# Kernel tuning notes

Hardware: AMD Instinct MI355X
Metric: run time of the kernel (lower is better)

The kernel has to match this reference:

```python
import jax, jax.numpy as jnp
import numpy as np

N, T, D = 128, 2048, 88

def setup_inputs() -> dict:
    key = jax.random.key(0)
    k1, k2 = jax.random.split(key)
    output = jax.random.normal(k1, (N, T, D), dtype=jnp.float32)
    # binary piano-roll style target (sparse note activations)
    target = (jax.random.uniform(k2, (N, T, D)) < 0.1).astype(jnp.float32)
    mask = jnp.ones((N, T), dtype=jnp.int32)  # left-aligned valid mask
    return {"output": output, "target": target, "mask": mask}

def reference(output, target, mask):
    # prediction = (sigmoid(output) > 0.5) -> non-differentiable 0/1 floats
    pred = (jax.nn.sigmoid(output) > 0.5).astype(output.dtype)
    # tru_pos summed over both feature and time dims -> [N]
    tru_pos = jnp.sum(pred * target, axis=(1, 2))
    # per-timestep false pos / false neg -> [N, T]
    false_pos = jnp.sum(pred * (1.0 - target), axis=2)
    false_neg = jnp.sum((1.0 - pred) * target, axis=2)
    # T_i = number of valid timesteps per sequence (loop runs over t < T_i)
    T_i = jnp.sum(mask, axis=1)  # [N] int
    valid = (jnp.arange(false_pos.shape[1])[None, :] < T_i[:, None]).astype(output.dtype)
    ratio = tru_pos[:, None] / (tru_pos[:, None] + false_pos + false_neg)  # [N, T]
    acc = jnp.sum(ratio * valid, axis=1) / T_i.astype(output.dtype)  # [N]
    return jnp.sum(acc)
```

## Files before the change

kernel.cpp:

```cpp
#include <hip/hip_runtime.h>
#include <stdint.h>

#define NN 128
#define TT 2048
#define DD 88
#define ROWS 32
#define F4_ROW 22
#define K1_BLOCKS (NN * TT / ROWS)
#define PARTS_PER_N (TT / ROWS)
#define CPN 8
#define K2_BLOCKS (NN * CPN)

typedef float f4 __attribute__((ext_vector_type(4)));

__global__ __launch_bounds__(256) void acc_rowstats_kernel(
    const float* __restrict__ outp, const float* __restrict__ tgt,
    float* __restrict__ fpfn, float* __restrict__ tp_part) {
  __shared__ float s_tp[4];

  const int tid = threadIdx.x;
  const int lane = tid & 63;
  const int wave = tid >> 6;
  const int blk = blockIdx.x;
  const size_t base = (size_t)blk * (ROWS * DD);

  const int r = tid >> 3;
  const int s = tid & 7;

  const f4* o4 = (const f4*)(outp + base) + (size_t)r * F4_ROW;
  const f4* g4 = (const f4*)(tgt + base) + (size_t)r * F4_ROW;

  const int j2 = (s < 6) ? (s + 16) : s;
  const f4 o0 = o4[s];
  const f4 g0 = g4[s];
  const f4 o1 = o4[s + 8];
  const f4 g1 = g4[s + 8];
  const f4 o2 = o4[j2];
  const f4 g2 = g4[j2];

  float x = 0.f, tp = 0.f;
  float x2 = 0.f, tp2 = 0.f;

#define ACC1(ov, gv, xa, ta)                        \
  do {                                              \
    const float pf = ((ov) > 0.f) ? 1.f : 0.f;      \
    (xa) += fabsf(pf - (gv));                       \
    (ta) = fmaf(pf, (gv), (ta));                    \
  } while (0)

  ACC1(o0.x, g0.x, x, tp); ACC1(o0.y, g0.y, x, tp);
  ACC1(o0.z, g0.z, x, tp); ACC1(o0.w, g0.w, x, tp);
  ACC1(o1.x, g1.x, x, tp); ACC1(o1.y, g1.y, x, tp);
  ACC1(o1.z, g1.z, x, tp); ACC1(o1.w, g1.w, x, tp);
  ACC1(o2.x, g2.x, x2, tp2); ACC1(o2.y, g2.y, x2, tp2);
  ACC1(o2.z, g2.z, x2, tp2); ACC1(o2.w, g2.w, x2, tp2);
#undef ACC1

  if (s < 6) { x += x2; tp += tp2; }

  x += __shfl_down(x, 4, 64);
  x += __shfl_down(x, 2, 64);
  x += __shfl_down(x, 1, 64);
  if (s == 0) fpfn[(size_t)blk * ROWS + r] = x;

  for (int off = 32; off > 0; off >>= 1) tp += __shfl_down(tp, off, 64);
  if (lane == 0) s_tp[wave] = tp;
  __syncthreads();
  if (tid == 0) tp_part[blk] = s_tp[0] + s_tp[1] + s_tp[2] + s_tp[3];
}

__global__ __launch_bounds__(256) void acc_chunk_kernel(
    const int* __restrict__ mask, const float* __restrict__ fpfn,
    const float* __restrict__ tp_part, float* __restrict__ accp) {
  const int b = blockIdx.x;
  const int n = b >> 3;
  const int c = b & (CPN - 1);
  const int tid = threadIdx.x;
  const int lane = tid & 63;
  const int wave = tid >> 6;
  __shared__ float s_ti[4];
  __shared__ float s_tp[4];
  __shared__ float s_a[4];

  const int4* m4 = (const int4*)(mask + (size_t)n * TT);
  const int4 v0 = m4[tid];
  const int4 v1 = m4[tid + 256];
  const float tpv = (tid < PARTS_PER_N) ? tp_part[n * PARTS_PER_N + tid] : 0.f;
  const int t = c * 256 + tid;
  const float fr = fpfn[(size_t)n * TT + t];

  int ti = v0.x + v0.y + v0.z + v0.w + v1.x + v1.y + v1.z + v1.w;
  float tp = tpv;
  for (int off = 32; off > 0; off >>= 1) {
    ti += __shfl_down(ti, off, 64);
    tp += __shfl_down(tp, off, 64);
  }
  if (lane == 0) { s_ti[wave] = (float)ti; s_tp[wave] = tp; }
  __syncthreads();
  const float fTi = s_ti[0] + s_ti[1] + s_ti[2] + s_ti[3];
  const float tpn = s_tp[0] + s_tp[1] + s_tp[2] + s_tp[3];
  const int Ti = (int)fTi;

  float a = (t < Ti) ? tpn / (tpn + fr) : 0.f;
  for (int off = 32; off > 0; off >>= 1) a += __shfl_down(a, off, 64);
  if (lane == 0) s_a[wave] = a;
  __syncthreads();
  if (tid == 0)
    accp[b] = (s_a[0] + s_a[1] + s_a[2] + s_a[3]) / fTi;
}

__global__ __launch_bounds__(256) void acc_sum_kernel(
    const float* __restrict__ accp, float* __restrict__ out) {
  const int tid = threadIdx.x;
  const int lane = tid & 63;
  const int wave = tid >> 6;
  __shared__ float s_a[4];
  float a = accp[tid] + accp[tid + 256] + accp[tid + 512] + accp[tid + 768];
  for (int off = 32; off > 0; off >>= 1) a += __shfl_down(a, off, 64);
  if (lane == 0) s_a[wave] = a;
  __syncthreads();
  if (tid == 0) out[0] = s_a[0] + s_a[1] + s_a[2] + s_a[3];
}

extern "C" void kernel_launch(void* const* d_in, const int* in_sizes, int n_in,
                              void* d_out, int out_size, void* d_ws, size_t ws_size,
                              hipStream_t stream) {
  const float* output = (const float*)d_in[0];
  const float* target = (const float*)d_in[1];
  const int* mask = (const int*)d_in[2];
  float* out = (float*)d_out;

  float* tp_part = (float*)d_ws;
  float* fpfn = tp_part + K1_BLOCKS;
  float* accp = fpfn + (size_t)NN * TT;

  acc_rowstats_kernel<<<K1_BLOCKS, 256, 0, stream>>>(output, target, fpfn, tp_part);
  acc_chunk_kernel<<<K2_BLOCKS, 256, 0, stream>>>(mask, fpfn, tp_part, accp);
  acc_sum_kernel<<<1, 256, 0, stream>>>(accp, out);
}
```

Baseline: 201.9 us.

## Process four tiles per block with double-buffered loads and per-wave TP partials

Each block of the row-stats kernel now handles four 32-row tiles instead of one. It software-pipelines the loads so the next tile's data is in flight while the current tile is reduced. The per-block shared-memory reduction and __syncthreads are dropped in favour of per-wave true-positive partials written to global memory, and the chunk kernel now reads 256 partials per sequence instead of 64. This cuts the block count and exposes more memory-level parallelism per thread, at the cost of more registers and a larger partial array.

```diff
diff --git a/kernel.cpp b/kernel.cpp
--- a/kernel.cpp
+++ b/kernel.cpp
@@ -6,8 +6,10 @@
 #define DD 88
 #define ROWS 32
 #define F4_ROW 22
-#define K1_BLOCKS (NN * TT / ROWS)
-#define PARTS_PER_N (TT / ROWS)
+#define TILES (NN * TT / ROWS)
+#define TILES_PER_BLK 4
+#define K1_GRID (TILES / TILES_PER_BLK)
+#define PARTS_PER_N 256
 #define CPN 8
 #define K2_BLOCKS (NN * CPN)
 
@@ -16,57 +18,65 @@
 __global__ __launch_bounds__(256) void acc_rowstats_kernel(
     const float* __restrict__ outp, const float* __restrict__ tgt,
     float* __restrict__ fpfn, float* __restrict__ tp_part) {
-  __shared__ float s_tp[4];
-
   const int tid = threadIdx.x;
   const int lane = tid & 63;
   const int wave = tid >> 6;
-  const int blk = blockIdx.x;
-  const size_t base = (size_t)blk * (ROWS * DD);
-
   const int r = tid >> 3;
   const int s = tid & 7;
+  const int j2 = (s < 6) ? (s + 16) : s;
+  const int tile0 = blockIdx.x * TILES_PER_BLK;
 
-  const f4* o4 = (const f4*)(outp + base) + (size_t)r * F4_ROW;
-  const f4* g4 = (const f4*)(tgt + base) + (size_t)r * F4_ROW;
+  const f4* __restrict__ ob = (const f4*)outp;
+  const f4* __restrict__ gb = (const f4*)tgt;
 
-  const int j2 = (s < 6) ? (s + 16) : s;
-  const f4 o0 = o4[s];
-  const f4 g0 = g4[s];
-  const f4 o1 = o4[s + 8];
-  const f4 g1 = g4[s + 8];
-  const f4 o2 = o4[j2];
-  const f4 g2 = g4[j2];
-
-  float x = 0.f, tp = 0.f;
-  float x2 = 0.f, tp2 = 0.f;
-
-#define ACC1(ov, gv, xa, ta)                        \
-  do {                                              \
-    const float pf = ((ov) > 0.f) ? 1.f : 0.f;      \
-    (xa) += fabsf(pf - (gv));                       \
-    (ta) = fmaf(pf, (gv), (ta));                    \
+#define LOADT(T, oA, gA, oB, gB, oC, gC)              \
+  do {                                                \
+    const size_t ro = ((size_t)(T) * ROWS + r) * F4_ROW; \
+    oA = ob[ro + s];      gA = gb[ro + s];            \
+    oB = ob[ro + s + 8];  gB = gb[ro + s + 8];        \
+    oC = ob[ro + j2];     gC = gb[ro + j2];           \
   } while (0)
 
-  ACC1(o0.x, g0.x, x, tp); ACC1(o0.y, g0.y, x, tp);
-  ACC1(o0.z, g0.z, x, tp); ACC1(o0.w, g0.w, x, tp);
-  ACC1(o1.x, g1.x, x, tp); ACC1(o1.y, g1.y, x, tp);
-  ACC1(o1.z, g1.z, x, tp); ACC1(o1.w, g1.w, x, tp);
-  ACC1(o2.x, g2.x, x2, tp2); ACC1(o2.y, g2.y, x2, tp2);
-  ACC1(o2.z, g2.z, x2, tp2); ACC1(o2.w, g2.w, x2, tp2);
+#define ACC1(ov, gv, xa, ta)                          \
+  do {                                                \
+    const float pf = ((ov) > 0.f) ? 1.f : 0.f;        \
+    (xa) += fabsf(pf - (gv));                         \
+    (ta) = fmaf(pf, (gv), (ta));                      \
+  } while (0)
+
+#define COMPT(T, oA, gA, oB, gB, oC, gC)                                   \
+  do {                                                                     \
+    float x = 0.f, tp = 0.f, x2 = 0.f, tp2 = 0.f;                          \
+    ACC1(oA.x, gA.x, x, tp);   ACC1(oA.y, gA.y, x, tp);                    \
+    ACC1(oA.z, gA.z, x, tp);   ACC1(oA.w, gA.w, x, tp);                    \
+    ACC1(oB.x, gB.x, x, tp);   ACC1(oB.y, gB.y, x, tp);                    \
+    ACC1(oB.z, gB.z, x, tp);   ACC1(oB.w, gB.w, x, tp);                    \
+    ACC1(oC.x, gC.x, x2, tp2); ACC1(oC.y, gC.y, x2, tp2);                  \
+    ACC1(oC.z, gC.z, x2, tp2); ACC1(oC.w, gC.w, x2, tp2);                  \
+    if (s < 6) { x += x2; tp += tp2; }                                     \
+    x += __shfl_down(x, 4, 64);                                            \
+    x += __shfl_down(x, 2, 64);                                            \
+    x += __shfl_down(x, 1, 64);                                            \
+    if (s == 0) fpfn[(size_t)(T)*ROWS + r] = x;                            \
+    for (int off = 32; off > 0; off >>= 1) tp += __shfl_down(tp, off, 64); \
+    if (lane == 0) tp_part[(size_t)(T)*4 + wave] = tp;                     \
+  } while (0)
+
+  f4 oA0, gA0, oB0, gB0, oC0, gC0;
+  f4 oA1, gA1, oB1, gB1, oC1, gC1;
+
+  LOADT(tile0 + 0, oA0, gA0, oB0, gB0, oC0, gC0);
+  LOADT(tile0 + 1, oA1, gA1, oB1, gB1, oC1, gC1);
+  COMPT(tile0 + 0, oA0, gA0, oB0, gB0, oC0, gC0);
+  LOADT(tile0 + 2, oA0, gA0, oB0, gB0, oC0, gC0);
+  COMPT(tile0 + 1, oA1, gA1, oB1, gB1, oC1, gC1);
+  LOADT(tile0 + 3, oA1, gA1, oB1, gB1, oC1, gC1);
+  COMPT(tile0 + 2, oA0, gA0, oB0, gB0, oC0, gC0);
+  COMPT(tile0 + 3, oA1, gA1, oB1, gB1, oC1, gC1);
+
+#undef LOADT
 #undef ACC1
-
-  if (s < 6) { x += x2; tp += tp2; }
-
-  x += __shfl_down(x, 4, 64);
-  x += __shfl_down(x, 2, 64);
-  x += __shfl_down(x, 1, 64);
-  if (s == 0) fpfn[(size_t)blk * ROWS + r] = x;
-
-  for (int off = 32; off > 0; off >>= 1) tp += __shfl_down(tp, off, 64);
-  if (lane == 0) s_tp[wave] = tp;
-  __syncthreads();
-  if (tid == 0) tp_part[blk] = s_tp[0] + s_tp[1] + s_tp[2] + s_tp[3];
+#undef COMPT
 }
 
 __global__ __launch_bounds__(256) void acc_chunk_kernel(
@@ -85,7 +95,7 @@
   const int4* m4 = (const int4*)(mask + (size_t)n * TT);
   const int4 v0 = m4[tid];
   const int4 v1 = m4[tid + 256];
-  const float tpv = (tid < PARTS_PER_N) ? tp_part[n * PARTS_PER_N + tid] : 0.f;
+  const float tpv = tp_part[n * PARTS_PER_N + tid];
   const int t = c * 256 + tid;
   const float fr = fpfn[(size_t)n * TT + t];
 
@@ -131,10 +141,10 @@
   float* out = (float*)d_out;
 
   float* tp_part = (float*)d_ws;
-  float* fpfn = tp_part + K1_BLOCKS;
+  float* fpfn = tp_part + (size_t)TILES * 4;
   float* accp = fpfn + (size_t)NN * TT;
 
-  acc_rowstats_kernel<<<K1_BLOCKS, 256, 0, stream>>>(output, target, fpfn, tp_part);
+  acc_rowstats_kernel<<<K1_GRID, 256, 0, stream>>>(output, target, fpfn, tp_part);
   acc_chunk_kernel<<<K2_BLOCKS, 256, 0, stream>>>(mask, fpfn, tp_part, accp);
   acc_sum_kernel<<<1, 256, 0, stream>>>(accp, out);
 }
```

Measured after the change: 204.8 us. No clear change (+1.4%).
